# Kernel optimization log

Hardware: AMD Instinct MI355X
Metric: run time of the kernel (lower is better)

Reference implementation:

```python
import jax, jax.numpy as jnp
import numpy as np

HEAD_DIM = 128
N_HEADS = 32
N_KV_HEADS = 8
EPS = 1e-6
ROPE_THETA = 1e6
NEG_INF = -1e9


def _rms_norm(x, w):
    # per-head RMSNorm over last dim (head_dim), fp32 math like Qwen3RMSNorm
    xf = x.astype(jnp.float32)
    var = jnp.mean(xf * xf, axis=-1, keepdims=True)
    return (w * (xf * jax.lax.rsqrt(var + EPS))).astype(x.dtype)


def _rope_cos_sin(position_ids, dtype):
    # default rope: inv_freq = theta^(-2i/d), emb = cat(freqs, freqs)
    inv_freq = 1.0 / (ROPE_THETA ** (jnp.arange(0, HEAD_DIM, 2, dtype=jnp.float32) / HEAD_DIM))
    freqs = position_ids.astype(jnp.float32)[:, :, None] * inv_freq[None, None, :]  # [B,S,hd/2]
    emb = jnp.concatenate([freqs, freqs], axis=-1)  # [B,S,hd]
    return jnp.cos(emb).astype(dtype), jnp.sin(emb).astype(dtype)


def _rotate_half(x):
    x1, x2 = jnp.split(x, 2, axis=-1)
    return jnp.concatenate([-x2, x1], axis=-1)


def setup_inputs() -> dict:
    key = jax.random.key(0)
    ks = jax.random.split(key, 6)
    B, S, H = 1, 2048, 4096
    return {
        "hidden_states": jax.random.normal(ks[0], (B, S, H), jnp.float32),
        "position_ids": jnp.broadcast_to(jnp.arange(S, dtype=jnp.int32)[None, :], (B, S)),
        "Wq": jax.random.normal(ks[1], (N_HEADS * HEAD_DIM, H), jnp.float32) * 0.02,
        "Wk": jax.random.normal(ks[2], (N_KV_HEADS * HEAD_DIM, H), jnp.float32) * 0.02,
        "Wv": jax.random.normal(ks[3], (N_KV_HEADS * HEAD_DIM, H), jnp.float32) * 0.02,
        "Wo": jax.random.normal(ks[4], (H, N_HEADS * HEAD_DIM), jnp.float32) * 0.02,
        "q_norm_w": jnp.ones((HEAD_DIM,), jnp.float32),
        "k_norm_w": jnp.ones((HEAD_DIM,), jnp.float32),
    }


def reference(hidden_states, position_ids, Wq, Wk, Wv, Wo, q_norm_w, k_norm_w):
    B, S, H = hidden_states.shape
    scaling = HEAD_DIM ** -0.5
    n_rep = N_HEADS // N_KV_HEADS

    # projections (torch Linear: y = x @ W.T), reshape to [B, heads, S, hd]
    q = jnp.einsum('bsh,dh->bsd', hidden_states, Wq).reshape(B, S, N_HEADS, HEAD_DIM)
    k = jnp.einsum('bsh,dh->bsd', hidden_states, Wk).reshape(B, S, N_KV_HEADS, HEAD_DIM)
    v = jnp.einsum('bsh,dh->bsd', hidden_states, Wv).reshape(B, S, N_KV_HEADS, HEAD_DIM)

    q = _rms_norm(q, q_norm_w).transpose(0, 2, 1, 3)  # [B,nH,S,hd]
    k = _rms_norm(k, k_norm_w).transpose(0, 2, 1, 3)  # [B,nKV,S,hd]
    v = v.transpose(0, 2, 1, 3)

    cos, sin = _rope_cos_sin(position_ids, hidden_states.dtype)
    cos = cos[:, None, :, :]  # unsqueeze head dim
    sin = sin[:, None, :, :]
    q = q * cos + _rotate_half(q) * sin
    k = k * cos + _rotate_half(k) * sin

    # GQA repeat_kv
    k = jnp.repeat(k, n_rep, axis=1)
    v = jnp.repeat(v, n_rep, axis=1)

    scores = jnp.einsum('bhqd,bhkd->bhqk', q, k) * scaling
    causal = jnp.where(
        jnp.arange(S)[:, None] >= jnp.arange(S)[None, :], 0.0, NEG_INF
    ).astype(scores.dtype)
    scores = scores + causal[None, None, :, :]
    attn = jax.nn.softmax(scores.astype(jnp.float32), axis=-1).astype(q.dtype)

    out = jnp.einsum('bhqk,bhkd->bhqd', attn, v)
    out = out.transpose(0, 2, 1, 3).reshape(B, S, N_HEADS * HEAD_DIM)
    return jnp.einsum('bsd,hd->bsh', out, Wo)
```

## Files before the change

### kernel.cpp

```cpp
#include <hip/hip_runtime.h>
#include <hip/hip_bf16.h>

typedef unsigned short u16;
typedef __bf16 bf16x8 __attribute__((ext_vector_type(8)));
typedef u16 u16x4 __attribute__((ext_vector_type(4)));
typedef u16 u16x8 __attribute__((ext_vector_type(8)));
typedef float f32x4 __attribute__((ext_vector_type(4)));

#define S_LEN  2048
#define HID    4096
#define NHEADS 32
#define NKV    8
#define HD     128
#define QDIM   (NHEADS*HD)
#define KVDIM  (NKV*HD)
#define NT     (S_LEN/64)

__device__ __forceinline__ u16 f2bf(float f) {
  unsigned u = __float_as_uint(f);
  u += 0x7fff + ((u >> 16) & 1);
  return (u16)(u >> 16);
}
__device__ __forceinline__ void lds_load16(const u16* g, u16* l) {
  __builtin_amdgcn_global_load_lds(
      (__attribute__((address_space(1))) void*)(g),
      (__attribute__((address_space(3))) void*)(l), 16, 0, 0);
}

__global__ __launch_bounds__(256) void f2b4(
    const float* __restrict__ s0, u16* __restrict__ d0, long n0,
    const float* __restrict__ s1, u16* __restrict__ d1, long n1,
    const float* __restrict__ s2, u16* __restrict__ d2, long n2,
    const float* __restrict__ s3, u16* __restrict__ d3, long n3)
{
  const float* s; u16* d; long n; int b0, nb;
  const int b = blockIdx.x;
  if (b < 1024)      { s=s0; d=d0; n=n0; b0=0;    nb=1024; }
  else if (b < 3072) { s=s1; d=d1; n=n1; b0=1024; nb=2048; }
  else if (b < 3584) { s=s2; d=d2; n=n2; b0=3072; nb=512;  }
  else               { s=s3; d=d3; n=n3; b0=3584; nb=512;  }
  long i = (long)(b - b0)*256 + threadIdx.x;
  const long stride = (long)nb*256;
  for (; i < n; i += stride) {
    f32x4 a = ((const f32x4*)s)[i*2];
    f32x4 c = ((const f32x4*)s)[i*2 + 1];
    u16x8 o;
    #pragma unroll
    for (int j = 0; j < 4; ++j) { o[j] = f2bf(a[j]); o[4+j] = f2bf(c[j]); }
    ((u16x8*)d)[i] = o;
  }
}

__global__ __launch_bounds__(256) void f2b(
    const float* __restrict__ in, u16* __restrict__ out, long n8)
{
  long i = (long)blockIdx.x * blockDim.x + threadIdx.x;
  const long stride = (long)gridDim.x * blockDim.x;
  for (; i < n8; i += stride) {
    f32x4 a = ((const f32x4*)in)[i*2];
    f32x4 b = ((const f32x4*)in)[i*2 + 1];
    u16x8 o;
    #pragma unroll
    for (int j = 0; j < 4; ++j) { o[j] = f2bf(a[j]); o[4+j] = f2bf(b[j]); }
    ((u16x8*)out)[i] = o;
  }
}

__global__ __launch_bounds__(512, 2) void gemmQ(
    const u16* __restrict__ A, const u16* __restrict__ B,
    u16* __restrict__ Cq, u16* __restrict__ Ck, u16* __restrict__ Cv,
    int K)
{
  __shared__ u16 lds[57344];
  const int tid  = threadIdx.x;
  const int lane = tid & 63;
  const int w    = tid >> 6;
  const int wr   = w >> 2, wc = w & 3;
  const int l16  = lane & 15, lhi = lane >> 4;
  const long arow0 = (long)blockIdx.y * 256;
  const long brow0 = (long)blockIdx.x * 192;
  const int ntiles = K >> 6;

  const int cu = ((lane & 7) ^ (lane >> 3)) * 8;
  const int wl = w*8 + (lane >> 3);
  const u16* Ag[4];
  #pragma unroll
  for (int r = 0; r < 4; ++r)
    Ag[r] = A + (arow0 + r*64 + wl)*(long)K + cu;
  const u16* Bg[3];
  #pragma unroll
  for (int r = 0; r < 2; ++r) {
    const int rp = r*64 + wl;
    Bg[r] = B + (brow0 + (rp >> 5)*48 + (rp & 31))*(long)K + cu;
  }
  Bg[2] = B + (brow0 + (wl >> 4)*48 + 32 + (wl & 15))*(long)K + cu;

  auto stageA = [&](int s, int kt) {
    u16* d = lds + ((kt & 1) << 14) + w*512;
    lds_load16(Ag[s]   + (long)kt*64, d + s*4096);
    lds_load16(Ag[s+2] + (long)kt*64, d + (s+2)*4096);
  };
  auto stageB0 = [&](int kt) {
    u16* d = lds + 32768 + (kt & 1)*12288 + w*512;
    lds_load16(Bg[0] + (long)kt*64, d);
    lds_load16(Bg[1] + (long)kt*64, d + 4096);
  };
  auto stageB1 = [&](int kt) {
    u16* d = lds + 32768 + (kt & 1)*12288 + w*512;
    lds_load16(Bg[2] + (long)kt*64, d + 8192);
  };

  const int xr = (l16 & 7) << 3;
  int offA[4][2], offB[2][2], offB2[2];
  #pragma unroll
  for (int m2 = 0; m2 < 4; ++m2)
    #pragma unroll
    for (int ks = 0; ks < 2; ++ks)
      offA[m2][ks] = (wr*128 + m2*16 + l16)*64 + ((ks*32 + lhi*8) ^ xr);
  #pragma unroll
  for (int n2 = 0; n2 < 2; ++n2)
    #pragma unroll
    for (int ks = 0; ks < 2; ++ks)
      offB[n2][ks] = (wc*32 + n2*16 + l16)*64 + ((ks*32 + lhi*8) ^ xr);
  #pragma unroll
  for (int ks = 0; ks < 2; ++ks)
    offB2[ks] = 8192 + (wc*16 + l16)*64 + ((ks*32 + lhi*8) ^ xr);

  f32x4 acc[8][3] = {};

  stageA(0, 0); stageB0(0); stageB1(0); stageA(1, 0);
  stageA(0, 1); stageB0(1); stageB1(1);
  asm volatile("s_waitcnt vmcnt(5)" ::: "memory");
  __builtin_amdgcn_s_barrier();

  #pragma unroll 2
  for (int t = 0; t < ntiles; ++t) {
    const int Ab = (t & 1) << 14;
    const int Bb = 32768 + (t & 1)*12288;
    bf16x8 af[4][2], af2[4][2], bf[2][2], bf2[2];

    #pragma unroll
    for (int m2 = 0; m2 < 4; ++m2)
      #pragma unroll
      for (int ks = 0; ks < 2; ++ks)
        af[m2][ks] = *(const bf16x8*)(lds + Ab + offA[m2][ks]);
    #pragma unroll
    for (int n2 = 0; n2 < 2; ++n2)
      #pragma unroll
      for (int ks = 0; ks < 2; ++ks)
        bf[n2][ks] = *(const bf16x8*)(lds + Bb + offB[n2][ks]);
    if (t + 1 < ntiles) stageA(1, t + 1);
    __builtin_amdgcn_s_barrier();
    asm volatile("s_waitcnt lgkmcnt(0)" ::: "memory");
    __builtin_amdgcn_s_setprio(1);
    #pragma unroll
    for (int m2 = 0; m2 < 4; ++m2)
      #pragma unroll
      for (int n2 = 0; n2 < 2; ++n2)
        #pragma unroll
        for (int ks = 0; ks < 2; ++ks)
          acc[m2][n2] = __builtin_amdgcn_mfma_f32_16x16x32_bf16(
              af[m2][ks], bf[n2][ks], acc[m2][n2], 0, 0, 0);
    __builtin_amdgcn_s_setprio(0);
    __builtin_amdgcn_s_barrier();

    #pragma unroll
    for (int ks = 0; ks < 2; ++ks)
      bf2[ks] = *(const bf16x8*)(lds + Bb + offB2[ks]);
    if (t + 2 < ntiles) stageA(0, t + 2);
    __builtin_amdgcn_s_barrier();
    asm volatile("s_waitcnt lgkmcnt(0)" ::: "memory");
    __builtin_amdgcn_s_setprio(1);
    #pragma unroll
    for (int m2 = 0; m2 < 4; ++m2)
      #pragma unroll
      for (int ks = 0; ks < 2; ++ks)
        acc[m2][2] = __builtin_amdgcn_mfma_f32_16x16x32_bf16(
            af[m2][ks], bf2[ks], acc[m2][2], 0, 0, 0);
    __builtin_amdgcn_s_setprio(0);
    __builtin_amdgcn_s_barrier();

    #pragma unroll
    for (int m2 = 0; m2 < 4; ++m2)
      #pragma unroll
      for (int ks = 0; ks < 2; ++ks)
        af2[m2][ks] = *(const bf16x8*)(lds + Ab + 4096 + offA[m2][ks]);
    if (t + 2 < ntiles) stageB0(t + 2);
    __builtin_amdgcn_s_barrier();
    asm volatile("s_waitcnt lgkmcnt(0)" ::: "memory");
    __builtin_amdgcn_s_setprio(1);
    #pragma unroll
    for (int m2 = 0; m2 < 4; ++m2)
      #pragma unroll
      for (int ks = 0; ks < 2; ++ks)
        acc[4+m2][2] = __builtin_amdgcn_mfma_f32_16x16x32_bf16(
            af2[m2][ks], bf2[ks], acc[4+m2][2], 0, 0, 0);
    __builtin_amdgcn_s_setprio(0);
    __builtin_amdgcn_s_barrier();

    if (t + 2 < ntiles) stageB1(t + 2);
    __builtin_amdgcn_s_barrier();
    __builtin_amdgcn_s_setprio(1);
    #pragma unroll
    for (int m2 = 0; m2 < 4; ++m2)
      #pragma unroll
      for (int n2 = 0; n2 < 2; ++n2)
        #pragma unroll
        for (int ks = 0; ks < 2; ++ks)
          acc[4+m2][n2] = __builtin_amdgcn_mfma_f32_16x16x32_bf16(
              af2[m2][ks], bf[n2][ks], acc[4+m2][n2], 0, 0, 0);
    __builtin_amdgcn_s_setprio(0);
    if (t + 2 < ntiles) { asm volatile("s_waitcnt vmcnt(5)" ::: "memory"); }
    else                { asm volatile("s_waitcnt vmcnt(0)" ::: "memory"); }
    __builtin_amdgcn_s_barrier();
  }

  #pragma unroll
  for (int m = 0; m < 8; ++m) {
    const long row = arow0 + wr*128 + (m >> 2)*64 + (m & 3)*16 + lhi*4;
    #pragma unroll
    for (int n = 0; n < 3; ++n) {
      const long col = brow0 + wc*48 + n*16 + l16;
      if (col < QDIM) {
        #pragma unroll
        for (int r = 0; r < 4; ++r)
          Cq[(row + r)*QDIM + col] = f2bf(acc[m][n][r]);
      } else if (col < QDIM + KVDIM) {
        #pragma unroll
        for (int r = 0; r < 4; ++r)
          Ck[(row + r)*KVDIM + (col - QDIM)] = f2bf(acc[m][n][r]);
      } else {
        u16x4 o;
        #pragma unroll
        for (int r = 0; r < 4; ++r) o[r] = f2bf(acc[m][n][r]);
        *(u16x4*)(Cv + (col - QDIM - KVDIM)*(long)S_LEN + row) = o;
      }
    }
  }
}

__global__ __launch_bounds__(512, 2) void gemmF(
    const u16* __restrict__ A, const u16* __restrict__ B,
    float* __restrict__ C, int M, int N, int K)
{
  __shared__ u16 lds[49152];
  const int tid  = threadIdx.x;
  const int lane = tid & 63;
  const int w    = tid >> 6;
  const int wr   = w >> 2, wc = w & 3;
  const int l16  = lane & 15, lhi = lane >> 4;
  const long arow0 = (long)blockIdx.y * 128;
  const long brow0 = (long)blockIdx.x * 256;
  const int ntiles = K >> 6;

  const int cu = ((lane & 7) ^ (lane >> 3)) * 8;
  const int rA  = (w >> 2)*64 + (w & 3)*8;
  const int rB1c = 128 + (w >> 2)*64 + (w & 3)*8;
  const u16* srcA  = A + (arow0 + rA   + (lane >> 3))*(long)K + cu;
  const u16* srcB0 = B + (brow0 + rA   + (lane >> 3))*(long)K + cu;
  const u16* srcB1 = B + (brow0 + rB1c + (lane >> 3))*(long)K + cu;
  u16* const dA  = lds + rA*64;
  u16* const dB0 = lds + 16384 + rA*64;
  u16* const dB1 = lds + 16384 + rB1c*64;

  auto stageA = [&](int s, int kt) {
    lds_load16(srcA + (long)(s*32)*K + kt*64,
               dA + ((kt & 1) << 13) + s*2048);
  };
  auto stageB = [&](int s, int kt) {
    const long so = (long)(s*32)*K + kt*64;
    const int  d  = ((kt & 1) << 14) + s*2048;
    lds_load16(srcB0 + so, dB0 + d);
    lds_load16(srcB1 + so, dB1 + d);
  };

  const int xr = (l16 & 7) << 3;
  int offA[2][2], offB[2][2];
  #pragma unroll
  for (int m = 0; m < 2; ++m)
    #pragma unroll
    for (int ks = 0; ks < 2; ++ks)
      offA[m][ks] = (wr*64 + m*16 + l16)*64 + ((ks*32 + lhi*8) ^ xr);
  #pragma unroll
  for (int n = 0; n < 2; ++n)
    #pragma unroll
    for (int ks = 0; ks < 2; ++ks)
      offB[n][ks] = (wc*64 + n*16 + l16)*64 + ((ks*32 + lhi*8) ^ xr);

  f32x4 acc[4][4] = {};

  stageA(0, 0); stageA(1, 0); stageB(0, 0); stageB(1, 0);
  if (ntiles > 1) { stageA(0, 1); stageB(0, 1); stageB(1, 1); }
  asm volatile("s_waitcnt vmcnt(5)" ::: "memory");
  __builtin_amdgcn_s_barrier();

  #pragma unroll 2
  for (int t = 0; t < ntiles; ++t) {
    const int Ab = (t & 1) << 13;
    const int Bb = 16384 + ((t & 1) << 14);
    bf16x8 af[2][2], bf[2][2], af2[2][2], bf2[2][2];

    #pragma unroll
    for (int m = 0; m < 2; ++m)
      #pragma unroll
      for (int ks = 0; ks < 2; ++ks)
        af[m][ks] = *(const bf16x8*)(lds + Ab + offA[m][ks]);
    #pragma unroll
    for (int n = 0; n < 2; ++n)
      #pragma unroll
      for (int ks = 0; ks < 2; ++ks)
        bf[n][ks] = *(const bf16x8*)(lds + Bb + offB[n][ks]);
    if (t + 1 < ntiles) stageA(1, t + 1);
    __builtin_amdgcn_s_barrier();
    asm volatile("s_waitcnt lgkmcnt(0)" ::: "memory");
    __builtin_amdgcn_s_setprio(1);
    #pragma unroll
    for (int m = 0; m < 2; ++m)
      #pragma unroll
      for (int n = 0; n < 2; ++n)
        #pragma unroll
        for (int ks = 0; ks < 2; ++ks)
          acc[m][n] = __builtin_amdgcn_mfma_f32_16x16x32_bf16(
              af[m][ks], bf[n][ks], acc[m][n], 0, 0, 0);
    __builtin_amdgcn_s_setprio(0);
    __builtin_amdgcn_s_barrier();

    #pragma unroll
    for (int n = 0; n < 2; ++n)
      #pragma unroll
      for (int ks = 0; ks < 2; ++ks)
        bf2[n][ks] = *(const bf16x8*)(lds + Bb + 2048 + offB[n][ks]);
    if (t + 2 < ntiles) stageA(0, t + 2);
    __builtin_amdgcn_s_barrier();
    asm volatile("s_waitcnt lgkmcnt(0)" ::: "memory");
    __builtin_amdgcn_s_setprio(1);
    #pragma unroll
    for (int m = 0; m < 2; ++m)
      #pragma unroll
      for (int n = 0; n < 2; ++n)
        #pragma unroll
        for (int ks = 0; ks < 2; ++ks)
          acc[m][2+n] = __builtin_amdgcn_mfma_f32_16x16x32_bf16(
              af[m][ks], bf2[n][ks], acc[m][2+n], 0, 0, 0);
    __builtin_amdgcn_s_setprio(0);
    __builtin_amdgcn_s_barrier();

    #pragma unroll
    for (int m = 0; m < 2; ++m)
      #pragma unroll
      for (int ks = 0; ks < 2; ++ks)
        af2[m][ks] = *(const bf16x8*)(lds + Ab + 2048 + offA[m][ks]);
    if (t + 2 < ntiles) stageB(0, t + 2);
    __builtin_amdgcn_s_barrier();
    asm volatile("s_waitcnt lgkmcnt(0)" ::: "memory");
    __builtin_amdgcn_s_setprio(1);
    #pragma unroll
    for (int m = 0; m < 2; ++m)
      #pragma unroll
      for (int n = 0; n < 2; ++n)
        #pragma unroll
        for (int ks = 0; ks < 2; ++ks)
          acc[2+m][2+n] = __builtin_amdgcn_mfma_f32_16x16x32_bf16(
              af2[m][ks], bf2[n][ks], acc[2+m][2+n], 0, 0, 0);
    __builtin_amdgcn_s_setprio(0);
    __builtin_amdgcn_s_barrier();

    if (t + 2 < ntiles) stageB(1, t + 2);
    __builtin_amdgcn_s_barrier();
    __builtin_amdgcn_s_setprio(1);
    #pragma unroll
    for (int m = 0; m < 2; ++m)
      #pragma unroll
      for (int n = 0; n < 2; ++n)
        #pragma unroll
        for (int ks = 0; ks < 2; ++ks)
          acc[2+m][n] = __builtin_amdgcn_mfma_f32_16x16x32_bf16(
              af2[m][ks], bf[n][ks], acc[2+m][n], 0, 0, 0);
    __builtin_amdgcn_s_setprio(0);
    if (t + 2 < ntiles) { asm volatile("s_waitcnt vmcnt(5)" ::: "memory"); }
    else                { asm volatile("s_waitcnt vmcnt(0)" ::: "memory"); }
    __builtin_amdgcn_s_barrier();
  }

  #pragma unroll
  for (int mi = 0; mi < 4; ++mi) {
    const long row = arow0 + wr*64 + (mi >> 1)*32 + (mi & 1)*16 + lhi*4;
    #pragma unroll
    for (int ni = 0; ni < 4; ++ni) {
      const long col = brow0 + wc*64 + (ni >> 1)*32 + (ni & 1)*16 + l16;
      #pragma unroll
      for (int r = 0; r < 4; ++r)
        C[(row + r)*N + col] = acc[mi][ni][r];
    }
  }
}

__global__ __launch_bounds__(256) void norm_rope2(
    u16* __restrict__ Qb, u16* __restrict__ Kb,
    const float* __restrict__ qw, const float* __restrict__ kw,
    const int* __restrict__ pos)
{
  const int row  = blockIdx.x * 4 + (threadIdx.x >> 6);
  const int lane = threadIdx.x & 63;
  u16* p; const float* nw; float sc; int s;
  if (row < S_LEN*NHEADS) {
    p = Qb + (long)row * HD; nw = qw; sc = 0.08838834764831845f; s = row >> 5;
  } else {
    const int r2 = row - S_LEN*NHEADS;
    p = Kb + (long)r2 * HD; nw = kw; sc = 1.0f; s = r2 >> 3;
  }

  float x1 = __uint_as_float(((unsigned)p[lane]) << 16);
  float x2 = __uint_as_float(((unsigned)p[lane + 64]) << 16);
  float ss = x1*x1 + x2*x2;
  #pragma unroll
  for (int m = 32; m >= 1; m >>= 1) ss += __shfl_xor(ss, m);
  const float inv = rsqrtf(ss * (1.0f/128.0f) + 1e-6f);
  x1 *= inv * nw[lane];
  x2 *= inv * nw[lane + 64];

  const float inv_freq = expf(-(float)lane * (13.815510557964274f / 64.0f));
  const float ang = (float)pos[s] * inv_freq;
  float sn, cs;
  sincosf(ang, &sn, &cs);
  p[lane]      = f2bf((x1*cs - x2*sn) * sc);
  p[lane + 64] = f2bf((x2*cs + x1*sn) * sc);
}

__global__ __launch_bounds__(256, 4) void attn(
    const u16* __restrict__ Q, const u16* __restrict__ K,
    const u16* __restrict__ VT, u16* __restrict__ O)
{
  __shared__ u16 Ks[64*128];
  __shared__ u16 Vt[128*64];
  __shared__ u16 Ps[4*16*64];

  const int tid  = threadIdx.x;
  const int lane = tid & 63;
  const int w    = tid >> 6;
  const int l16  = lane & 15, lhi = lane >> 4;

  const int lid = ((blockIdx.x & 7) << 7) + (blockIdx.x >> 3);
  const int h   = lid >> 5;
  const int xx  = lid & 31;
  const int kh  = h >> 2;
  const int T   = (NT - 1) - ((xx + h) & (NT - 1));
  const int qrow0 = T*64 + w*16;

  bf16x8 qf[4];
  #pragma unroll
  for (int ks = 0; ks < 4; ++ks)
    qf[ks] = *(const bf16x8*)(Q + (long)(qrow0 + l16)*QDIM + h*HD + ks*32 + lhi*8);

  float mr[4] = {-1e30f,-1e30f,-1e30f,-1e30f};
  float lr[4] = {0.f,0.f,0.f,0.f};
  f32x4 of[8] = {};
  u16* Pw = Ps + w*16*64;

  for (int t = 0; t <= T; ++t) {
    const int kv0 = t * 64;
    #pragma unroll
    for (int i = 0; i < 4; ++i) {
      const int r   = w*16 + i*4 + lhi;
      const int col = (l16*8) ^ ((r & 7) << 3);
      lds_load16(K + (long)(kv0 + r)*KVDIM + kh*HD + col,
                 Ks + (w*16 + i*4)*128);
    }
    #pragma unroll
    for (int i = 0; i < 4; ++i) {
      const int r   = w*32 + i*8 + (lane >> 3);
      const int col = ((lane & 7)*8) ^ ((r & 7) << 3);
      lds_load16(VT + (long)(kh*HD + r)*S_LEN + kv0 + col,
                 Vt + (w*32 + i*8)*64);
    }
    __syncthreads();

    f32x4 sa[4] = {};
    __builtin_amdgcn_s_setprio(1);
    #pragma unroll
    for (int n = 0; n < 4; ++n)
      #pragma unroll
      for (int ks = 0; ks < 4; ++ks) {
        bf16x8 kf = *(const bf16x8*)(
            Ks + (n*16 + l16)*128 + ((ks*32 + lhi*8) ^ ((l16 & 7) << 3)));
        sa[n] = __builtin_amdgcn_mfma_f32_16x16x32_bf16(qf[ks], kf, sa[n], 0, 0, 0);
      }
    __builtin_amdgcn_s_setprio(0);

    const bool diag = (t == T);
    float pm[4];
    #pragma unroll
    for (int r = 0; r < 4; ++r) {
      const int grow = qrow0 + lhi*4 + r;
      #pragma unroll
      for (int n = 0; n < 4; ++n) {
        float sv = sa[n][r];
        if (diag && (kv0 + n*16 + l16 > grow)) sv = -1e9f;
        sa[n][r] = sv;
      }
      float p01 = fmaxf(sa[0][r], sa[1][r]);
      float p23 = fmaxf(sa[2][r], sa[3][r]);
      float pmx = fmaxf(p01, p23);
      pmx = fmaxf(pmx, __shfl_xor(pmx, 1));
      pmx = fmaxf(pmx, __shfl_xor(pmx, 2));
      pmx = fmaxf(pmx, __shfl_xor(pmx, 4));
      pmx = fmaxf(pmx, __shfl_xor(pmx, 8));
      pm[r] = pmx;
    }
    bool need = (pm[0] > mr[0] + 8.f) | (pm[1] > mr[1] + 8.f) |
                (pm[2] > mr[2] + 8.f) | (pm[3] > mr[3] + 8.f);
    if (__any(need)) {
      #pragma unroll
      for (int r = 0; r < 4; ++r) {
        const float mnew  = fmaxf(mr[r], pm[r]);
        const float alpha = __expf(mr[r] - mnew);
        mr[r] = mnew;
        lr[r] *= alpha;
        #pragma unroll
        for (int c = 0; c < 8; ++c) of[c][r] *= alpha;
      }
    }
    #pragma unroll
    for (int r = 0; r < 4; ++r) {
      float rsum = 0.f;
      #pragma unroll
      for (int n = 0; n < 4; ++n) {
        float pv = __expf(sa[n][r] - mr[r]);
        sa[n][r] = pv;
        rsum += pv;
      }
      rsum += __shfl_xor(rsum, 1);
      rsum += __shfl_xor(rsum, 2);
      rsum += __shfl_xor(rsum, 4);
      rsum += __shfl_xor(rsum, 8);
      lr[r] += rsum;
    }

    #pragma unroll
    for (int r = 0; r < 4; ++r) {
      const int prow = lhi*4 + r;
      #pragma unroll
      for (int n = 0; n < 4; ++n)
        Pw[prow*64 + ((n*16 + l16) ^ ((prow & 7) << 3))] = f2bf(sa[n][r]);
    }
    __builtin_amdgcn_s_setprio(1);
    #pragma unroll
    for (int ks = 0; ks < 2; ++ks) {
      bf16x8 pf = *(const bf16x8*)(
          Pw + l16*64 + ((ks*32 + lhi*8) ^ ((l16 & 7) << 3)));
      #pragma unroll
      for (int c = 0; c < 8; ++c) {
        bf16x8 vf = *(const bf16x8*)(
            Vt + (c*16 + l16)*64 + ((ks*32 + lhi*8) ^ ((l16 & 7) << 3)));
        of[c] = __builtin_amdgcn_mfma_f32_16x16x32_bf16(pf, vf, of[c], 0, 0, 0);
      }
    }
    __builtin_amdgcn_s_setprio(0);
    __syncthreads();
  }

  #pragma unroll
  for (int r = 0; r < 4; ++r) {
    const float invl = 1.0f / lr[r];
    const long orow = (long)(qrow0 + lhi*4 + r) * QDIM + h*HD;
    #pragma unroll
    for (int c = 0; c < 8; ++c)
      O[orow + c*16 + l16] = f2bf(of[c][r] * invl);
  }
}

extern "C" void kernel_launch(void* const* d_in, const int* in_sizes, int n_in,
                              void* d_out, int out_size, void* d_ws, size_t ws_size,
                              hipStream_t stream) {
  (void)in_sizes; (void)n_in; (void)out_size; (void)ws_size;
  const float* hs  = (const float*)d_in[0];
  const int*   pos = (const int*)d_in[1];
  const float* Wq  = (const float*)d_in[2];
  const float* Wk  = (const float*)d_in[3];
  const float* Wv  = (const float*)d_in[4];
  const float* Wo  = (const float*)d_in[5];
  const float* qw  = (const float*)d_in[6];
  const float* kw  = (const float*)d_in[7];

  u16* hsB = (u16*)d_ws;
  u16* W1  = hsB + (long)S_LEN*HID;
  u16* WkB = W1  + (long)QDIM*HID;
  u16* WvB = WkB + (long)KVDIM*HID;
  u16* Kb  = WvB + (long)KVDIM*HID;
  u16* VT  = Kb  + (long)S_LEN*KVDIM;
  u16* AO  = VT  + (long)KVDIM*S_LEN;
  u16* Qb  = (u16*)d_out;

  f2b4<<<4096, 256, 0, stream>>>(hs, hsB, (long)S_LEN*HID/8,
                                 Wq, W1,  (long)QDIM*HID/8,
                                 Wk, WkB, (long)KVDIM*HID/8,
                                 Wv, WvB, (long)KVDIM*HID/8);

  gemmQ<<<dim3((QDIM+2*KVDIM)/192, S_LEN/256), 512, 0, stream>>>(
      hsB, W1, Qb, Kb, VT, HID);

  norm_rope2<<<(S_LEN*NHEADS + S_LEN*NKV)/4, 256, 0, stream>>>(
      Qb, Kb, qw, kw, pos);

  f2b<<<2048, 256, 0, stream>>>(Wo, W1, (long)HID*QDIM/8);

  attn<<<dim3(NT*NHEADS), 256, 0, stream>>>(Qb, Kb, VT, AO);

  gemmF<<<dim3(HID/256, S_LEN/128), 512, 0, stream>>>(
      AO, W1, (float*)d_out, S_LEN, HID, QDIM);
}
```

Measured before the change: 371.5 us.

## Split long causal attention query tiles across two blocks with merge kernel

Attention blocks for the upper 16 query tiles are now split into two halves along the KV range. Each half writes unnormalized fp32 partial outputs plus row max and sum into reused workspace buffers, and a new merge kernel combines them. The aim is to balance work across blocks and shorten the critical path of causal attention. The cost is an extra kernel launch and extra fp32 partial traffic, and it relies on reusing the hsB/WkB buffers and the region past Q in the output buffer as scratch.

```diff
diff --git a/kernel.cpp b/kernel.cpp
--- a/kernel.cpp
+++ b/kernel.cpp
@@ -429,7 +429,8 @@
 
 __global__ __launch_bounds__(256, 4) void attn(
     const u16* __restrict__ Q, const u16* __restrict__ K,
-    const u16* __restrict__ VT, u16* __restrict__ O)
+    const u16* __restrict__ VT, u16* __restrict__ O,
+    float* __restrict__ OP0, float* __restrict__ OP1, float* __restrict__ ML)
 {
   __shared__ u16 Ks[64*128];
   __shared__ u16 Vt[128*64];
@@ -440,12 +441,27 @@
   const int w    = tid >> 6;
   const int l16  = lane & 15, lhi = lane >> 4;
 
-  const int lid = ((blockIdx.x & 7) << 7) + (blockIdx.x >> 3);
-  const int h   = lid >> 5;
-  const int xx  = lid & 31;
-  const int kh  = h >> 2;
-  const int T   = (NT - 1) - ((xx + h) & (NT - 1));
-  const int qrow0 = T*64 + w*16;
+  const int bx = blockIdx.x;
+  int h, Tq, t0, t1;
+  bool split;
+  if (bx < 1024) {
+    const int pid  = bx >> 1;
+    const int half = bx & 1;
+    Tq = 31 - (pid >> 5);
+    h  = pid & 31;
+    const int nk = Tq + 1, nh = nk >> 1;
+    t0 = half ? nh : 0;
+    t1 = half ? nk : nh;
+    split = true;
+  } else {
+    const int s = bx - 1024;
+    Tq = 15 - (s >> 5);
+    h  = s & 31;
+    t0 = 0; t1 = Tq + 1;
+    split = false;
+  }
+  const int kh = h >> 2;
+  const int qrow0 = Tq*64 + w*16;
 
   bf16x8 qf[4];
   #pragma unroll
@@ -457,7 +473,7 @@
   f32x4 of[8] = {};
   u16* Pw = Ps + w*16*64;
 
-  for (int t = 0; t <= T; ++t) {
+  for (int t = t0; t < t1; ++t) {
     const int kv0 = t * 64;
     #pragma unroll
     for (int i = 0; i < 4; ++i) {
@@ -487,7 +503,7 @@
       }
     __builtin_amdgcn_s_setprio(0);
 
-    const bool diag = (t == T);
+    const bool diag = (t == Tq);
     float pm[4];
     #pragma unroll
     for (int r = 0; r < 4; ++r) {
@@ -559,14 +575,51 @@
     __syncthreads();
   }
 
-  #pragma unroll
-  for (int r = 0; r < 4; ++r) {
-    const float invl = 1.0f / lr[r];
-    const long orow = (long)(qrow0 + lhi*4 + r) * QDIM + h*HD;
-    #pragma unroll
-    for (int c = 0; c < 8; ++c)
-      O[orow + c*16 + l16] = f2bf(of[c][r] * invl);
-  }
+  if (split) {
+    float* Op = ((bx & 1) ? OP1 : OP0) + (long)(bx >> 1) * 8192;
+    #pragma unroll
+    for (int r = 0; r < 4; ++r) {
+      const int row = w*16 + lhi*4 + r;
+      #pragma unroll
+      for (int c = 0; c < 8; ++c)
+        Op[row*128 + c*16 + l16] = of[c][r];
+      if (l16 == 0) {
+        ML[(long)bx*128 + row*2]     = mr[r];
+        ML[(long)bx*128 + row*2 + 1] = lr[r];
+      }
+    }
+  } else {
+    #pragma unroll
+    for (int r = 0; r < 4; ++r) {
+      const float invl = 1.0f / lr[r];
+      const long orow = (long)(qrow0 + lhi*4 + r) * QDIM + h*HD;
+      #pragma unroll
+      for (int c = 0; c < 8; ++c)
+        O[orow + c*16 + l16] = f2bf(of[c][r] * invl);
+    }
+  }
+}
+
+__global__ __launch_bounds__(256) void mrg(
+    const float* __restrict__ OP0, const float* __restrict__ OP1,
+    const float* __restrict__ ML, u16* __restrict__ O)
+{
+  const int r0  = blockIdx.x*2 + (threadIdx.x >> 7);
+  const int pid = r0 >> 6;
+  const int row = r0 & 63;
+  const int d   = threadIdx.x & 127;
+  const int Tq  = 31 - (pid >> 5);
+  const int h   = pid & 31;
+  const long mb0 = (long)(2*pid)*128 + row*2;
+  const long mb1 = mb0 + 128;
+  const float m0 = ML[mb0],     l0 = ML[mb0 + 1];
+  const float m1 = ML[mb1],     l1 = ML[mb1 + 1];
+  const float m  = fmaxf(m0, m1);
+  const float a0 = __expf(m0 - m), a1 = __expf(m1 - m);
+  const float o0 = OP0[(long)pid*8192 + row*128 + d];
+  const float o1 = OP1[(long)pid*8192 + row*128 + d];
+  const float o  = (o0*a0 + o1*a1) / (l0*a0 + l1*a1);
+  O[(long)(Tq*64 + row)*QDIM + h*HD + d] = f2bf(o);
 }
 
 extern "C" void kernel_launch(void* const* d_in, const int* in_sizes, int n_in,
@@ -591,6 +644,10 @@
   u16* AO  = VT  + (long)KVDIM*S_LEN;
   u16* Qb  = (u16*)d_out;
 
+  float* OP0 = (float*)hsB;
+  float* OP1 = (float*)WkB;
+  float* ML  = (float*)(Qb + (long)S_LEN*QDIM);
+
   f2b4<<<4096, 256, 0, stream>>>(hs, hsB, (long)S_LEN*HID/8,
                                  Wq, W1,  (long)QDIM*HID/8,
                                  Wk, WkB, (long)KVDIM*HID/8,
@@ -604,7 +661,8 @@
 
   f2b<<<2048, 256, 0, stream>>>(Wo, W1, (long)HID*QDIM/8);
 
-  attn<<<dim3(NT*NHEADS), 256, 0, stream>>>(Qb, Kb, VT, AO);
+  attn<<<dim3(1536), 256, 0, stream>>>(Qb, Kb, VT, AO, OP0, OP1, ML);
+  mrg<<<dim3(16384), 256, 0, stream>>>(OP0, OP1, ML, AO);
 
   gemmF<<<dim3(HID/256, S_LEN/128), 512, 0, stream>>>(
       AO, W1, (float*)d_out, S_LEN, HID, QDIM);
```

Measured after the change: 361.1 us. -2.8%, faster.

## Balance causal attention by pairing query tiles and splitting long rows across blocks

Applied to the files above, without the earlier changes.

Attention blocks are reorganized: 512 blocks compute the first 16 KV tiles of long query tiles and write fp32 partial outputs plus max/sum stats, while another 512 blocks each handle one short tile (p) in full and then the remainder of a long tile (31-p), merging with the partial via a flag-based spin-wait. This evens out the per-block work of the causal triangle to reduce tail imbalance. It adds fp32 partial traffic through workspace, inter-block flag synchronization (deadlock risk if producers are not scheduled), and the GEMMs are templated on compile-time sizes.

```diff
diff --git a/kernel.cpp b/kernel.cpp
--- a/kernel.cpp
+++ b/kernel.cpp
@@ -52,8 +52,10 @@
 }
 
 __global__ __launch_bounds__(256) void f2b(
-    const float* __restrict__ in, u16* __restrict__ out, long n8)
+    const float* __restrict__ in, u16* __restrict__ out, long n8,
+    unsigned* __restrict__ flags)
 {
+  if (blockIdx.x == 0 && threadIdx.x < 512) flags[threadIdx.x] = 0u;
   long i = (long)blockIdx.x * blockDim.x + threadIdx.x;
   const long stride = (long)gridDim.x * blockDim.x;
   for (; i < n8; i += stride) {
@@ -66,10 +68,10 @@
   }
 }
 
+template<int K>
 __global__ __launch_bounds__(512, 2) void gemmQ(
     const u16* __restrict__ A, const u16* __restrict__ B,
-    u16* __restrict__ Cq, u16* __restrict__ Ck, u16* __restrict__ Cv,
-    int K)
+    u16* __restrict__ Cq, u16* __restrict__ Ck, u16* __restrict__ Cv)
 {
   __shared__ u16 lds[57344];
   const int tid  = threadIdx.x;
@@ -239,9 +241,10 @@
   }
 }
 
+template<int N, int K>
 __global__ __launch_bounds__(512, 2) void gemmF(
     const u16* __restrict__ A, const u16* __restrict__ B,
-    float* __restrict__ C, int M, int N, int K)
+    float* __restrict__ C)
 {
   __shared__ u16 lds[49152];
   const int tid  = threadIdx.x;
@@ -429,7 +432,9 @@
 
 __global__ __launch_bounds__(256, 4) void attn(
     const u16* __restrict__ Q, const u16* __restrict__ K,
-    const u16* __restrict__ VT, u16* __restrict__ O)
+    const u16* __restrict__ VT, u16* __restrict__ O,
+    float* __restrict__ OP0, float* __restrict__ ML,
+    unsigned* __restrict__ flags)
 {
   __shared__ u16 Ks[64*128];
   __shared__ u16 Vt[128*64];
@@ -440,132 +445,186 @@
   const int w    = tid >> 6;
   const int l16  = lane & 15, lhi = lane >> 4;
 
-  const int lid = ((blockIdx.x & 7) << 7) + (blockIdx.x >> 3);
-  const int h   = lid >> 5;
-  const int xx  = lid & 31;
-  const int kh  = h >> 2;
-  const int T   = (NT - 1) - ((xx + h) & (NT - 1));
-  const int qrow0 = T*64 + w*16;
-
-  bf16x8 qf[4];
-  #pragma unroll
-  for (int ks = 0; ks < 4; ++ks)
-    qf[ks] = *(const bf16x8*)(Q + (long)(qrow0 + l16)*QDIM + h*HD + ks*32 + lhi*8);
-
-  float mr[4] = {-1e30f,-1e30f,-1e30f,-1e30f};
-  float lr[4] = {0.f,0.f,0.f,0.f};
-  f32x4 of[8] = {};
-  u16* Pw = Ps + w*16*64;
-
-  for (int t = 0; t <= T; ++t) {
-    const int kv0 = t * 64;
-    #pragma unroll
-    for (int i = 0; i < 4; ++i) {
-      const int r   = w*16 + i*4 + lhi;
-      const int col = (l16*8) ^ ((r & 7) << 3);
-      lds_load16(K + (long)(kv0 + r)*KVDIM + kh*HD + col,
-                 Ks + (w*16 + i*4)*128);
+  const int bx   = blockIdx.x;
+  const int role = bx >> 9;
+  const int a    = bx & 511;
+  const int kh   = a & 7;
+  const int jj   = (a >> 3) & 3;
+  const int p    = a >> 5;
+  const int h    = kh*4 + jj;
+  const int pid  = h*16 + p;
+  const int hi   = 31 - p;
+
+  const int nseg = role ? 2 : 1;
+  for (int sg = 0; sg < nseg; ++sg) {
+    const int qt  = (role && sg == 0) ? p : hi;
+    const int tt0 = (role && sg == 1) ? 16 : 0;
+    const int tt1 = role ? (sg ? hi + 1 : p + 1) : 16;
+    const int qrow0 = qt*64 + w*16;
+
+    bf16x8 qf[4];
+    #pragma unroll
+    for (int ks = 0; ks < 4; ++ks)
+      qf[ks] = *(const bf16x8*)(Q + (long)(qrow0 + l16)*QDIM + h*HD + ks*32 + lhi*8);
+
+    float mr[4] = {-1e30f,-1e30f,-1e30f,-1e30f};
+    float lr[4] = {0.f,0.f,0.f,0.f};
+    f32x4 of[8] = {};
+    u16* Pw = Ps + w*16*64;
+
+    for (int t = tt0; t < tt1; ++t) {
+      const int kv0 = t * 64;
+      #pragma unroll
+      for (int i = 0; i < 4; ++i) {
+        const int r   = w*16 + i*4 + lhi;
+        const int col = (l16*8) ^ ((r & 7) << 3);
+        lds_load16(K + (long)(kv0 + r)*KVDIM + kh*HD + col,
+                   Ks + (w*16 + i*4)*128);
+      }
+      #pragma unroll
+      for (int i = 0; i < 4; ++i) {
+        const int r   = w*32 + i*8 + (lane >> 3);
+        const int col = ((lane & 7)*8) ^ ((r & 7) << 3);
+        lds_load16(VT + (long)(kh*HD + r)*S_LEN + kv0 + col,
+                   Vt + (w*32 + i*8)*64);
+      }
+      __syncthreads();
+
+      f32x4 sa[4] = {};
+      __builtin_amdgcn_s_setprio(1);
+      #pragma unroll
+      for (int n = 0; n < 4; ++n)
+        #pragma unroll
+        for (int ks = 0; ks < 4; ++ks) {
+          bf16x8 kf = *(const bf16x8*)(
+              Ks + (n*16 + l16)*128 + ((ks*32 + lhi*8) ^ ((l16 & 7) << 3)));
+          sa[n] = __builtin_amdgcn_mfma_f32_16x16x32_bf16(qf[ks], kf, sa[n], 0, 0, 0);
+        }
+      __builtin_amdgcn_s_setprio(0);
+
+      const bool diag = (t == qt);
+      float pm[4];
+      #pragma unroll
+      for (int r = 0; r < 4; ++r) {
+        const int grow = qrow0 + lhi*4 + r;
+        #pragma unroll
+        for (int n = 0; n < 4; ++n) {
+          float sv = sa[n][r];
+          if (diag && (kv0 + n*16 + l16 > grow)) sv = -1e9f;
+          sa[n][r] = sv;
+        }
+        float p01 = fmaxf(sa[0][r], sa[1][r]);
+        float p23 = fmaxf(sa[2][r], sa[3][r]);
+        float pmx = fmaxf(p01, p23);
+        pmx = fmaxf(pmx, __shfl_xor(pmx, 1));
+        pmx = fmaxf(pmx, __shfl_xor(pmx, 2));
+        pmx = fmaxf(pmx, __shfl_xor(pmx, 4));
+        pmx = fmaxf(pmx, __shfl_xor(pmx, 8));
+        pm[r] = pmx;
+      }
+      bool need = (pm[0] > mr[0] + 8.f) | (pm[1] > mr[1] + 8.f) |
+                  (pm[2] > mr[2] + 8.f) | (pm[3] > mr[3] + 8.f);
+      if (__any(need)) {
+        #pragma unroll
+        for (int r = 0; r < 4; ++r) {
+          const float mnew  = fmaxf(mr[r], pm[r]);
+          const float alpha = __expf(mr[r] - mnew);
+          mr[r] = mnew;
+          lr[r] *= alpha;
+          #pragma unroll
+          for (int c = 0; c < 8; ++c) of[c][r] *= alpha;
+        }
+      }
+      #pragma unroll
+      for (int r = 0; r < 4; ++r) {
+        float rsum = 0.f;
+        #pragma unroll
+        for (int n = 0; n < 4; ++n) {
+          float pv = __expf(sa[n][r] - mr[r]);
+          sa[n][r] = pv;
+          rsum += pv;
+        }
+        rsum += __shfl_xor(rsum, 1);
+        rsum += __shfl_xor(rsum, 2);
+        rsum += __shfl_xor(rsum, 4);
+        rsum += __shfl_xor(rsum, 8);
+        lr[r] += rsum;
+      }
+
+      #pragma unroll
+      for (int r = 0; r < 4; ++r) {
+        const int prow = lhi*4 + r;
+        #pragma unroll
+        for (int n = 0; n < 4; ++n)
+          Pw[prow*64 + ((n*16 + l16) ^ ((prow & 7) << 3))] = f2bf(sa[n][r]);
+      }
+      __builtin_amdgcn_s_setprio(1);
+      #pragma unroll
+      for (int ks = 0; ks < 2; ++ks) {
+        bf16x8 pf = *(const bf16x8*)(
+            Pw + l16*64 + ((ks*32 + lhi*8) ^ ((l16 & 7) << 3)));
+        #pragma unroll
+        for (int c = 0; c < 8; ++c) {
+          bf16x8 vf = *(const bf16x8*)(
+              Vt + (c*16 + l16)*64 + ((ks*32 + lhi*8) ^ ((l16 & 7) << 3)));
+          of[c] = __builtin_amdgcn_mfma_f32_16x16x32_bf16(pf, vf, of[c], 0, 0, 0);
+        }
+      }
+      __builtin_amdgcn_s_setprio(0);
+      __syncthreads();
     }
-    #pragma unroll
-    for (int i = 0; i < 4; ++i) {
-      const int r   = w*32 + i*8 + (lane >> 3);
-      const int col = ((lane & 7)*8) ^ ((r & 7) << 3);
-      lds_load16(VT + (long)(kh*HD + r)*S_LEN + kv0 + col,
-                 Vt + (w*32 + i*8)*64);
+
+    if (!role) {
+      float* Op = OP0 + (long)pid * 8192;
+      #pragma unroll
+      for (int r = 0; r < 4; ++r) {
+        const int row = w*16 + lhi*4 + r;
+        #pragma unroll
+        for (int c = 0; c < 8; ++c)
+          Op[row*128 + c*16 + l16] = of[c][r];
+        if (l16 == 0) {
+          ML[pid*128 + row*2]     = mr[r];
+          ML[pid*128 + row*2 + 1] = lr[r];
+        }
+      }
+      asm volatile("s_waitcnt vmcnt(0)" ::: "memory");
+      __syncthreads();
+      if (tid == 0)
+        __hip_atomic_store(&flags[pid], 1u, __ATOMIC_RELEASE,
+                           __HIP_MEMORY_SCOPE_AGENT);
+    } else if (sg == 0) {
+      #pragma unroll
+      for (int r = 0; r < 4; ++r) {
+        const float invl = 1.0f / lr[r];
+        const long orow = (long)(qrow0 + lhi*4 + r) * QDIM + h*HD;
+        #pragma unroll
+        for (int c = 0; c < 8; ++c)
+          O[orow + c*16 + l16] = f2bf(of[c][r] * invl);
+      }
+    } else {
+      if (lane == 0) {
+        while (__hip_atomic_load(&flags[pid], __ATOMIC_ACQUIRE,
+                                 __HIP_MEMORY_SCOPE_AGENT) == 0u)
+          __builtin_amdgcn_s_sleep(2);
+      }
+      __syncthreads();
+      const float* Op = OP0 + (long)pid * 8192;
+      #pragma unroll
+      for (int r = 0; r < 4; ++r) {
+        const int row = w*16 + lhi*4 + r;
+        const float mA = ML[pid*128 + row*2];
+        const float lA = ML[pid*128 + row*2 + 1];
+        const float m  = fmaxf(mA, mr[r]);
+        const float a0 = __expf(mA - m), a1 = __expf(mr[r] - m);
+        const float invl = 1.0f / (lA*a0 + lr[r]*a1);
+        const long orow = (long)(qrow0 + lhi*4 + r) * QDIM + h*HD;
+        #pragma unroll
+        for (int c = 0; c < 8; ++c) {
+          const float oA = Op[row*128 + c*16 + l16];
+          O[orow + c*16 + l16] = f2bf((oA*a0 + of[c][r]*a1) * invl);
+        }
+      }
     }
-    __syncthreads();
-
-    f32x4 sa[4] = {};
-    __builtin_amdgcn_s_setprio(1);
-    #pragma unroll
-    for (int n = 0; n < 4; ++n)
-      #pragma unroll
-      for (int ks = 0; ks < 4; ++ks) {
-        bf16x8 kf = *(const bf16x8*)(
-            Ks + (n*16 + l16)*128 + ((ks*32 + lhi*8) ^ ((l16 & 7) << 3)));
-        sa[n] = __builtin_amdgcn_mfma_f32_16x16x32_bf16(qf[ks], kf, sa[n], 0, 0, 0);
-      }
-    __builtin_amdgcn_s_setprio(0);
-
-    const bool diag = (t == T);
-    float pm[4];
-    #pragma unroll
-    for (int r = 0; r < 4; ++r) {
-      const int grow = qrow0 + lhi*4 + r;
-      #pragma unroll
-      for (int n = 0; n < 4; ++n) {
-        float sv = sa[n][r];
-        if (diag && (kv0 + n*16 + l16 > grow)) sv = -1e9f;
-        sa[n][r] = sv;
-      }
-      float p01 = fmaxf(sa[0][r], sa[1][r]);
-      float p23 = fmaxf(sa[2][r], sa[3][r]);
-      float pmx = fmaxf(p01, p23);
-      pmx = fmaxf(pmx, __shfl_xor(pmx, 1));
-      pmx = fmaxf(pmx, __shfl_xor(pmx, 2));
-      pmx = fmaxf(pmx, __shfl_xor(pmx, 4));
-      pmx = fmaxf(pmx, __shfl_xor(pmx, 8));
-      pm[r] = pmx;
-    }
-    bool need = (pm[0] > mr[0] + 8.f) | (pm[1] > mr[1] + 8.f) |
-                (pm[2] > mr[2] + 8.f) | (pm[3] > mr[3] + 8.f);
-    if (__any(need)) {
-      #pragma unroll
-      for (int r = 0; r < 4; ++r) {
-        const float mnew  = fmaxf(mr[r], pm[r]);
-        const float alpha = __expf(mr[r] - mnew);
-        mr[r] = mnew;
-        lr[r] *= alpha;
-        #pragma unroll
-        for (int c = 0; c < 8; ++c) of[c][r] *= alpha;
-      }
-    }
-    #pragma unroll
-    for (int r = 0; r < 4; ++r) {
-      float rsum = 0.f;
-      #pragma unroll
-      for (int n = 0; n < 4; ++n) {
-        float pv = __expf(sa[n][r] - mr[r]);
-        sa[n][r] = pv;
-        rsum += pv;
-      }
-      rsum += __shfl_xor(rsum, 1);
-      rsum += __shfl_xor(rsum, 2);
-      rsum += __shfl_xor(rsum, 4);
-      rsum += __shfl_xor(rsum, 8);
-      lr[r] += rsum;
-    }
-
-    #pragma unroll
-    for (int r = 0; r < 4; ++r) {
-      const int prow = lhi*4 + r;
-      #pragma unroll
-      for (int n = 0; n < 4; ++n)
-        Pw[prow*64 + ((n*16 + l16) ^ ((prow & 7) << 3))] = f2bf(sa[n][r]);
-    }
-    __builtin_amdgcn_s_setprio(1);
-    #pragma unroll
-    for (int ks = 0; ks < 2; ++ks) {
-      bf16x8 pf = *(const bf16x8*)(
-          Pw + l16*64 + ((ks*32 + lhi*8) ^ ((l16 & 7) << 3)));
-      #pragma unroll
-      for (int c = 0; c < 8; ++c) {
-        bf16x8 vf = *(const bf16x8*)(
-            Vt + (c*16 + l16)*64 + ((ks*32 + lhi*8) ^ ((l16 & 7) << 3)));
-        of[c] = __builtin_amdgcn_mfma_f32_16x16x32_bf16(pf, vf, of[c], 0, 0, 0);
-      }
-    }
-    __builtin_amdgcn_s_setprio(0);
-    __syncthreads();
-  }
-
-  #pragma unroll
-  for (int r = 0; r < 4; ++r) {
-    const float invl = 1.0f / lr[r];
-    const long orow = (long)(qrow0 + lhi*4 + r) * QDIM + h*HD;
-    #pragma unroll
-    for (int c = 0; c < 8; ++c)
-      O[orow + c*16 + l16] = f2bf(of[c][r] * invl);
   }
 }
 
@@ -591,21 +650,25 @@
   u16* AO  = VT  + (long)KVDIM*S_LEN;
   u16* Qb  = (u16*)d_out;
 
+  float*    OP0   = (float*)hsB;
+  float*    ML    = (float*)(Qb + (long)S_LEN*QDIM);
+  unsigned* flags = (unsigned*)(ML + 512*128);
+
   f2b4<<<4096, 256, 0, stream>>>(hs, hsB, (long)S_LEN*HID/8,
                                  Wq, W1,  (long)QDIM*HID/8,
                                  Wk, WkB, (long)KVDIM*HID/8,
                                  Wv, WvB, (long)KVDIM*HID/8);
 
-  gemmQ<<<dim3((QDIM+2*KVDIM)/192, S_LEN/256), 512, 0, stream>>>(
-      hsB, W1, Qb, Kb, VT, HID);
+  gemmQ<HID><<<dim3((QDIM+2*KVDIM)/192, S_LEN/256), 512, 0, stream>>>(
+      hsB, W1, Qb, Kb, VT);
 
   norm_rope2<<<(S_LEN*NHEADS + S_LEN*NKV)/4, 256, 0, stream>>>(
       Qb, Kb, qw, kw, pos);
 
-  f2b<<<2048, 256, 0, stream>>>(Wo, W1, (long)HID*QDIM/8);
-
-  attn<<<dim3(NT*NHEADS), 256, 0, stream>>>(Qb, Kb, VT, AO);
-
-  gemmF<<<dim3(HID/256, S_LEN/128), 512, 0, stream>>>(
-      AO, W1, (float*)d_out, S_LEN, HID, QDIM);
-}
+  f2b<<<2048, 256, 0, stream>>>(Wo, W1, (long)HID*QDIM/8, flags);
+
+  attn<<<dim3(1024), 256, 0, stream>>>(Qb, Kb, VT, AO, OP0, ML, flags);
+
+  gemmF<HID, QDIM><<<dim3(HID/256, S_LEN/128), 512, 0, stream>>>(
+      AO, W1, (float*)d_out);
+}
```

Result: faster. 357.4 us (-3.8%).
